# Kernel tuning notes

Measured on AMD Instinct MI355X. Metric: run time of the kernel, lower is better.

Reference implementation:

```python
import jax, jax.numpy as jnp
import numpy as np

N_NODES = 100000
N_REL = 8
N_EDGES = 80000
IN_F, HID, OUT = 128, 32, 2
N_GRAPHS = 64


def setup_inputs() -> dict:
    key = jax.random.key(0)
    ks = jax.random.split(key, 12)
    x = jax.random.normal(ks[0], (N_NODES, IN_F), dtype=jnp.float32)
    src = jax.random.randint(ks[1], (N_REL, N_EDGES), 0, N_NODES, dtype=jnp.int32)
    dst = jax.random.randint(ks[2], (N_REL, N_EDGES), 0, N_NODES, dtype=jnp.int32)
    graph_ids = jax.random.randint(ks[3], (N_NODES,), 0, N_GRAPHS, dtype=jnp.int32)
    W1 = jax.random.normal(ks[4], (N_REL, IN_F, HID), dtype=jnp.float32) / np.sqrt(IN_F)
    b1 = jnp.zeros((N_REL, HID), dtype=jnp.float32)
    W2 = jax.random.normal(ks[5], (N_REL, HID, HID), dtype=jnp.float32) / np.sqrt(HID)
    b2 = jnp.zeros((N_REL, HID), dtype=jnp.float32)
    Wc = jax.random.normal(ks[6], (HID, OUT), dtype=jnp.float32) / np.sqrt(HID)
    bc = jnp.zeros((OUT,), dtype=jnp.float32)
    return {"x": x, "src": src, "dst": dst, "graph_ids": graph_ids,
            "num_graphs": N_GRAPHS, "W1": W1, "b1": b1, "W2": W2, "b2": b2,
            "Wc": Wc, "bc": bc}


def _hetero_conv(h, src, dst, W, b, n_nodes):
    """HeteroGraphConv(sum) of per-relation GraphConv(norm='both')."""
    n_rel = W.shape[0]
    out = jnp.zeros((n_nodes, W.shape[2]), dtype=h.dtype)
    ones_e = jnp.ones((src.shape[1],), dtype=h.dtype)
    for r in range(n_rel):  # small fixed relation set
        s, d = src[r], dst[r]
        # symmetric normalization with degree clamped to >= 1 (DGL behavior)
        deg_out = jnp.maximum(jax.ops.segment_sum(ones_e, s, num_segments=n_nodes), 1.0)
        deg_in = jnp.maximum(jax.ops.segment_sum(ones_e, d, num_segments=n_nodes), 1.0)
        hn = h * jax.lax.rsqrt(deg_out)[:, None]      # [N, F_in]
        hw = hn @ W[r]                                # project first (F_in >= F_out)
        agg = jax.ops.segment_sum(hw[s], d, num_segments=n_nodes)  # scatter-sum to dst
        out = out + agg * jax.lax.rsqrt(deg_in)[:, None] + b[r]
    return out


def reference(x, src, dst, graph_ids, num_graphs, W1, b1, W2, b2, Wc, bc):
    n = x.shape[0]
    h = jax.nn.relu(_hetero_conv(x, src, dst, W1, b1, n))
    h = _hetero_conv(h, src, dst, W2, b2, n)
    # per-graph mean pooling over nodes
    sums = jax.ops.segment_sum(h, graph_ids, num_segments=num_graphs)
    cnts = jnp.maximum(jax.ops.segment_sum(jnp.ones((n,), h.dtype), graph_ids,
                                           num_segments=num_graphs), 1.0)
    pooled = sums / cnts[:, None]
    return pooled @ Wc + bc
```

## Files before the change

### kernel.cpp

```cpp
#include <hip/hip_runtime.h>


#define N_NODES 100000
#define N_REL   8
#define N_EDGES 80000
#define IN_F    128
#define HID     32
#define N_GRAPHS 64
#define NCAT    (N_REL * HID)
#define N_KEYS  (N_NODES * N_REL)
#define TOT_E   (N_REL * N_EDGES)
#define DRANGE  12500

constexpr int TILE = 256;
constexpr int KC   = 32;

typedef __attribute__((ext_vector_type(8))) short bf16x8;
typedef __attribute__((ext_vector_type(4))) float f32x4;

__device__ __forceinline__ ushort f2bf(float v) {
  unsigned u = __builtin_bit_cast(unsigned, v);
  u = (u + 0x7fffu + ((u >> 16) & 1u)) >> 16;
  return (ushort)u;
}
__device__ __forceinline__ float bf2f(ushort h) {
  unsigned u = ((unsigned)h) << 16;
  return __builtin_bit_cast(float, u);
}

__global__ __launch_bounds__(256) void deg_hist_kernel(const int* __restrict__ src, const int* __restrict__ dst,
                                                       int* __restrict__ dego, int* __restrict__ cnt) {
  int q = blockIdx.x & 7;
  int bb = blockIdx.x >> 3;
  int nb = gridDim.x >> 3;
  for (int i = bb * 256 + threadIdx.x; i < TOT_E; i += nb * 256) {
    int s = src[i], d = dst[i];
    int r = i / N_EDGES;
    if (s / DRANGE == q) atomicAdd(&dego[r * N_NODES + s], 1);
    if (d / DRANGE == q) atomicAdd(&cnt[d * N_REL + r], 1);
  }
}

__global__ __launch_bounds__(256) void rsqrt_kernel(float* __restrict__ p, int count) {
  int i = blockIdx.x * 256 + threadIdx.x;
  if (i < count) {
    int d = ((const int*)p)[i];
    p[i] = rsqrtf((float)(d < 1 ? 1 : d));
  }
}

__global__ __launch_bounds__(256) void prep_w_kernel(const float* __restrict__ W1, const float* __restrict__ W2,
                                                     const float* __restrict__ Wc,
                                                     ushort* __restrict__ Wt1, ushort* __restrict__ Vt) {
  int i = blockIdx.x * 256 + threadIdx.x;
  if (i < NCAT * IN_F) {
    int n = i >> 7, k = i & 127;
    int r = n >> 5, j = n & 31;
    Wt1[i] = f2bf(W1[r * (IN_F * HID) + k * HID + j]);
  } else {
    int q = i - NCAT * IN_F;
    if (q < 16 * HID) {
      int n = q >> 5, k = q & 31;
      int r = n >> 1, c = n & 1;
      float s = 0.f;
#pragma unroll
      for (int j = 0; j < HID; j++) s += W2[r * (HID * HID) + k * HID + j] * Wc[j * 2 + c];
      Vt[q] = f2bf(s);
    }
  }
}

__global__ __launch_bounds__(256) void scan1_kernel(const int* __restrict__ in, int* __restrict__ out,
                                                    int* __restrict__ partial, int n) {
  __shared__ int ts[256];
  int b0 = blockIdx.x * 1024;
  int t = threadIdx.x;
  int v[4]; int s = 0;
#pragma unroll
  for (int k = 0; k < 4; k++) {
    int idx = b0 + t * 4 + k;
    v[k] = s;
    s += (idx < n) ? in[idx] : 0;
  }
  ts[t] = s;
  __syncthreads();
  for (int off = 1; off < 256; off <<= 1) {
    int xv = (t >= off) ? ts[t - off] : 0;
    __syncthreads();
    ts[t] += xv;
    __syncthreads();
  }
  int texcl = (t == 0) ? 0 : ts[t - 1];
#pragma unroll
  for (int k = 0; k < 4; k++) {
    int idx = b0 + t * 4 + k;
    if (idx < n) out[idx] = texcl + v[k];
  }
  if (t == 255) partial[blockIdx.x] = ts[255];
}

__global__ __launch_bounds__(256) void scan2_kernel(int* __restrict__ partial, int nb) {
  __shared__ int ts[256];
  int t = threadIdx.x;
  int v[4]; int s = 0;
#pragma unroll
  for (int k = 0; k < 4; k++) {
    int idx = t * 4 + k;
    v[k] = s;
    s += (idx < nb) ? partial[idx] : 0;
  }
  ts[t] = s;
  __syncthreads();
  for (int off = 1; off < 256; off <<= 1) {
    int xv = (t >= off) ? ts[t - off] : 0;
    __syncthreads();
    ts[t] += xv;
    __syncthreads();
  }
  int texcl = (t == 0) ? 0 : ts[t - 1];
#pragma unroll
  for (int k = 0; k < 4; k++) {
    int idx = t * 4 + k;
    if (idx < nb) partial[idx] = texcl + v[k];
  }
}

__global__ __launch_bounds__(256) void scan3_kernel(int* __restrict__ out, const int* __restrict__ partial, int n) {
  int i = blockIdx.x * 256 + threadIdx.x;
  if (i < n) out[i] += partial[i >> 10];
  if (i == 0) out[n] = TOT_E;
}

__global__ __launch_bounds__(256) void fill_kernel(const int* __restrict__ src, const int* __restrict__ dst,
                                                   const int* __restrict__ rp, int* __restrict__ fillc,
                                                   const int* __restrict__ cnt,
                                                   int* __restrict__ ecol1, int* __restrict__ ecol2,
                                                   float* __restrict__ ew) {
  int q = blockIdx.x & 7;
  int bb = blockIdx.x >> 3;
  int nb = gridDim.x >> 3;
  for (int i = bb * 256 + threadIdx.x; i < TOT_E; i += nb * 256) {
    int d = dst[i];
    if (d / DRANGE != q) continue;
    int s = src[i];
    int r = i / N_EDGES;
    int key = d * N_REL + r;
    int c = cnt[key];
    int pos = atomicAdd(&fillc[key], 1);
    int t = rp[key] + pos;
    ecol1[t] = s * NCAT + r * HID;
    ecol2[t] = s * 16 + r * 2;
    ew[t] = rsqrtf((float)(c < 1 ? 1 : c));
  }
}

__global__ __launch_bounds__(256, 4) void gemm1_staged(const float* __restrict__ A, const ushort* __restrict__ Bt,
                                                       const float* __restrict__ rs_o, ushort* __restrict__ Y, int M) {
  __shared__ ushort smem[17408];
  int wave = __builtin_amdgcn_readfirstlane(threadIdx.x >> 6);
  int lane = threadIdx.x & 63;
  int t = threadIdx.x;
  int m0 = (blockIdx.x * 4 + wave) * 16;
  int me = (m0 <= M - 16) ? m0 : (M - 16);
  int row = lane & 15, quad = lane >> 4;

  bf16x8 af[4];
#pragma unroll
  for (int kq = 0; kq < 4; kq++) {
    const float* ap = &A[(size_t)(me + row) * IN_F + kq * 32 + quad * 8];
    float4 a0 = *(const float4*)ap;
    float4 a1 = *(const float4*)(ap + 4);
    bf16x8 a;
    a[0] = (short)f2bf(a0.x); a[1] = (short)f2bf(a0.y); a[2] = (short)f2bf(a0.z); a[3] = (short)f2bf(a0.w);
    a[4] = (short)f2bf(a1.x); a[5] = (short)f2bf(a1.y); a[6] = (short)f2bf(a1.z); a[7] = (short)f2bf(a1.w);
    af[kq] = a;
  }

  f32x4 acc[16];
#pragma unroll
  for (int nt = 0; nt < 16; nt++) acc[nt] = (f32x4){0.f, 0.f, 0.f, 0.f};

  for (int p = 0; p < 2; p++) {
    __syncthreads();
    const ushort* bsrc = Bt + (size_t)p * (128 * IN_F);
#pragma unroll
    for (int i = 0; i < 8; i++) {
      int c = t + i * 256;
      int rr2 = c >> 4, cc = c & 15;
      uint4 v = *(const uint4*)&bsrc[rr2 * IN_F + cc * 8];
      *(uint4*)&smem[rr2 * 136 + cc * 8] = v;
    }
    __syncthreads();
#pragma unroll
    for (int kq = 0; kq < 4; kq++) {
#pragma unroll
      for (int nt2 = 0; nt2 < 8; nt2++) {
        bf16x8 b = *(const bf16x8*)&smem[(nt2 * 16 + row) * 136 + kq * 32 + quad * 8];
        acc[p * 8 + nt2] = __builtin_amdgcn_mfma_f32_16x16x32_bf16(af[kq], b, acc[p * 8 + nt2], 0, 0, 0);
      }
    }
  }
  __syncthreads();

  float4 sc[N_REL];
#pragma unroll
  for (int r = 0; r < N_REL; r++)
    sc[r] = *(const float4*)&rs_o[(size_t)r * N_NODES + me + quad * 4];
  ushort* myt = &smem[wave * 4160];
#pragma unroll
  for (int nt = 0; nt < 16; nt++) {
    const float* s4 = (const float*)&sc[nt >> 1];
#pragma unroll
    for (int i = 0; i < 4; i++)
      myt[(quad * 4 + i) * 260 + nt * 16 + row] = f2bf(acc[nt][i] * s4[i]);
  }
  if (m0 <= M - 16) {
    ushort* ybase = &Y[(size_t)m0 * NCAT];
#pragma unroll
    for (int k = 0; k < 8; k++) {
      int g = k * 512 + lane * 8;
      int r2 = g >> 8, c2 = g & 255;
      const ushort* sp = &myt[r2 * 260 + c2];
      uint4 v;
      v.x = *(const uint*)(sp + 0);
      v.y = *(const uint*)(sp + 2);
      v.z = *(const uint*)(sp + 4);
      v.w = *(const uint*)(sp + 6);
      *(uint4*)&ybase[g] = v;
    }
  }
}

__global__ __launch_bounds__(256) void gemm2_mfma(const ushort* __restrict__ H, const ushort* __restrict__ Vt,
                                                  const float* __restrict__ rs_o, float* __restrict__ Ys2, int M) {
  int wave = __builtin_amdgcn_readfirstlane(threadIdx.x >> 6);
  int lane = threadIdx.x & 63;
  int m0 = (blockIdx.x * 4 + wave) * 16;
  if (m0 >= M) return;
  int row = lane & 15, quad = lane >> 4;
  f32x4 acc = (f32x4){0.f, 0.f, 0.f, 0.f};
  bf16x8 a = *(const bf16x8*)&H[(size_t)(m0 + row) * HID + quad * 8];
  bf16x8 b = *(const bf16x8*)&Vt[row * HID + quad * 8];
  acc = __builtin_amdgcn_mfma_f32_16x16x32_bf16(a, b, acc, 0, 0, 0);
  int r = row >> 1;
#pragma unroll
  for (int i = 0; i < 4; i++) {
    int m = m0 + quad * 4 + i;
    Ys2[(size_t)m * 16 + row] = acc[i] * rs_o[(size_t)r * N_NODES + m];
  }
}

__global__ __launch_bounds__(256) void gather1_kernel(const ushort* __restrict__ Ys, const int* __restrict__ ecol1,
                                                      const float* __restrict__ ew, const int* __restrict__ rp,
                                                      const float* __restrict__ b1, ushort* __restrict__ H) {
  int wave = __builtin_amdgcn_readfirstlane(threadIdx.x >> 6);
  int lane = threadIdx.x & 63;
  int d = blockIdx.x * 4 + wave;
  if (d >= N_NODES) return;
  int j = lane & 31, half = lane >> 5;
  int base = rp[d * N_REL], endp = rp[d * N_REL + N_REL];
  float sum = 0.f;
  for (int t = base + half; t < endp; t += 2) {
    int off = ecol1[t];
    float w = ew[t];
    sum += w * bf2f(Ys[(size_t)off + j]);
  }
  sum += __shfl_down(sum, 32);
  if (half == 0) {
    float sb = 0.f;
#pragma unroll
    for (int q = 0; q < N_REL; q++) sb += b1[q * HID + j];
    H[(size_t)d * HID + j] = f2bf(fmaxf(sum + sb, 0.f));
  }
}

__global__ __launch_bounds__(256) void gather2_pool_kernel(const float* __restrict__ Ys2,
                                                           const int* __restrict__ ecol2,
                                                           const float* __restrict__ ew, const int* __restrict__ rp,
                                                           const int* __restrict__ gid,
                                                           float* __restrict__ gpool, float* __restrict__ gcnt) {
  __shared__ float lp[N_GRAPHS * 2];
  __shared__ float lc[N_GRAPHS];
  int t = threadIdx.x;
  if (t < N_GRAPHS * 2) lp[t] = 0.f;
  if (t < N_GRAPHS) lc[t] = 0.f;
  __syncthreads();
  for (int n = blockIdx.x * 256 + t; n < N_NODES; n += gridDim.x * 256) {
    int base = rp[n * N_REL], endp = rp[n * N_REL + N_REL];
    float z0 = 0.f, z1 = 0.f;
    for (int s = base; s < endp; s++) {
      float w = ew[s];
      float2 y = *(const float2*)&Ys2[ecol2[s]];
      z0 += w * y.x;
      z1 += w * y.y;
    }
    int g = gid[n];
    atomicAdd(&lp[g * 2 + 0], z0);
    atomicAdd(&lp[g * 2 + 1], z1);
    atomicAdd(&lc[g], 1.f);
  }
  __syncthreads();
  if (t < N_GRAPHS * 2) atomicAdd(&gpool[t], lp[t]);
  if (t < N_GRAPHS) atomicAdd(&gcnt[t], lc[t]);
}

__global__ void final_kernel(const float* __restrict__ gpool, const float* __restrict__ gcnt,
                             const float* __restrict__ b2, const float* __restrict__ Wc,
                             const float* __restrict__ bc, float* __restrict__ out) {
  int g = threadIdx.x;
  if (g >= N_GRAPHS) return;
  float c0 = 0.f, c1 = 0.f;
#pragma unroll
  for (int k = 0; k < HID; k++) {
    float sb = 0.f;
#pragma unroll
    for (int r = 0; r < N_REL; r++) sb += b2[r * HID + k];
    c0 += sb * Wc[k * 2 + 0];
    c1 += sb * Wc[k * 2 + 1];
  }
  float cntv = gcnt[g];
  if (cntv > 0.f) {
    out[g * 2 + 0] = gpool[g * 2 + 0] / cntv + c0 + bc[0];
    out[g * 2 + 1] = gpool[g * 2 + 1] / cntv + c1 + bc[1];
  } else {
    out[g * 2 + 0] = bc[0];
    out[g * 2 + 1] = bc[1];
  }
}

__global__ __launch_bounds__(256) void deg_kernel(const int* __restrict__ src, const int* __restrict__ dst,
                                                  int* __restrict__ dego, int* __restrict__ degi, int n_rel) {
  int i = blockIdx.x * 256 + threadIdx.x;
  if (i < n_rel * N_EDGES) {
    int r = i / N_EDGES;
    atomicAdd(&dego[r * N_NODES + src[i]], 1);
    atomicAdd(&degi[r * N_NODES + dst[i]], 1);
  }
}

__global__ __launch_bounds__(256) void proj1_kernel(const float* __restrict__ x, const float* __restrict__ W1r0,
                                                    const float* __restrict__ rs_o, float* __restrict__ hw,
                                                    int n0, int n1, int hw_nodes) {
  int rr = blockIdx.y;
  int nb = n0 + blockIdx.x * TILE;
  int t = threadIdx.x;
  __shared__ float xs[TILE][KC + 4];
  const float* __restrict__ Wr = W1r0 + (size_t)rr * (IN_F * HID);
  float acc[HID];
#pragma unroll
  for (int j = 0; j < HID; j++) acc[j] = 0.f;
  for (int kc = 0; kc < IN_F; kc += KC) {
    __syncthreads();
#pragma unroll
    for (int i = 0; i < (TILE * KC / 4) / 256; i++) {
      int q = t + i * 256;
      int nn = q >> 3, k4 = q & 7;
      int n = nb + nn;
      float4 v = make_float4(0.f, 0.f, 0.f, 0.f);
      if (n < n1) v = *(const float4*)&x[(size_t)n * IN_F + kc + k4 * 4];
      *(float4*)&xs[nn][k4 * 4] = v;
    }
    __syncthreads();
#pragma unroll
    for (int k4 = 0; k4 < KC / 4; k4++) {
      float4 xv = *(const float4*)&xs[t][k4 * 4];
      const float* wk = &Wr[(kc + k4 * 4) * HID];
#pragma unroll
      for (int j = 0; j < HID; j++) acc[j] += xv.x * wk[j];
#pragma unroll
      for (int j = 0; j < HID; j++) acc[j] += xv.y * wk[HID + j];
#pragma unroll
      for (int j = 0; j < HID; j++) acc[j] += xv.z * wk[2 * HID + j];
#pragma unroll
      for (int j = 0; j < HID; j++) acc[j] += xv.w * wk[3 * HID + j];
    }
  }
  int n = nb + t;
  if (n < n1) {
    float s = rs_o[(size_t)rr * N_NODES + n];
    float* o = &hw[((size_t)rr * hw_nodes + (n - n0)) * HID];
#pragma unroll
    for (int j4 = 0; j4 < HID / 4; j4++) {
      float4 v = make_float4(acc[j4 * 4] * s, acc[j4 * 4 + 1] * s, acc[j4 * 4 + 2] * s, acc[j4 * 4 + 3] * s);
      *(float4*)&o[j4 * 4] = v;
    }
  }
}

__global__ __launch_bounds__(256) void proj2_kernel(const float* __restrict__ acc1, const float* __restrict__ b1,
                                                    const float* __restrict__ W2r0, const float* __restrict__ rs_o,
                                                    float* __restrict__ hw, int n0, int n1, int hw_nodes) {
  int n = n0 + blockIdx.x * 256 + threadIdx.x;
  if (n >= n1) return;
  int rr = blockIdx.y;
  float h1[HID];
#pragma unroll
  for (int j4 = 0; j4 < HID / 4; j4++) {
    float4 v = *(const float4*)&acc1[(size_t)n * HID + j4 * 4];
    h1[j4 * 4 + 0] = v.x; h1[j4 * 4 + 1] = v.y; h1[j4 * 4 + 2] = v.z; h1[j4 * 4 + 3] = v.w;
  }
#pragma unroll
  for (int j = 0; j < HID; j++) {
    float sb = 0.f;
#pragma unroll
    for (int q = 0; q < N_REL; q++) sb += b1[q * HID + j];
    h1[j] = fmaxf(h1[j] + sb, 0.f);
  }
  const float* __restrict__ Wr = W2r0 + (size_t)rr * (HID * HID);
  float acc[HID];
#pragma unroll
  for (int j = 0; j < HID; j++) acc[j] = 0.f;
#pragma unroll
  for (int k = 0; k < HID; k++) {
    float hv = h1[k];
#pragma unroll
    for (int j = 0; j < HID; j++) acc[j] += hv * Wr[k * HID + j];
  }
  float s = rs_o[(size_t)rr * N_NODES + n];
  float* o = &hw[((size_t)rr * hw_nodes + (n - n0)) * HID];
#pragma unroll
  for (int j4 = 0; j4 < HID / 4; j4++) {
    float4 v = make_float4(acc[j4 * 4] * s, acc[j4 * 4 + 1] * s, acc[j4 * 4 + 2] * s, acc[j4 * 4 + 3] * s);
    *(float4*)&o[j4 * 4] = v;
  }
}

__global__ __launch_bounds__(256) void scatter_kernel(const float* __restrict__ hw, const int* __restrict__ src,
                                                      const int* __restrict__ dst, const float* __restrict__ rs_i,
                                                      float* __restrict__ acc, int nr, int n0, int n1, int hw_nodes) {
  long i = (long)blockIdx.x * 256 + threadIdx.x;
  long total = (long)nr * N_EDGES * HID;
  if (i >= total) return;
  int j = (int)(i & (HID - 1));
  long e = i >> 5;
  int rr = (int)(e / N_EDGES);
  int ee = (int)(e - (long)rr * N_EDGES);
  int s = src[rr * N_EDGES + ee];
  if (s < n0 || s >= n1) return;
  int d = dst[rr * N_EDGES + ee];
  float v = hw[((size_t)rr * hw_nodes + (s - n0)) * HID + j] * rs_i[(size_t)rr * N_NODES + d];
  atomicAdd(&acc[(size_t)d * HID + j], v);
}

__global__ __launch_bounds__(256) void pool_kernel(const float* __restrict__ acc2, const float* __restrict__ b2,
                                                   const int* __restrict__ gid, float* __restrict__ gpool,
                                                   float* __restrict__ gcnt) {
  __shared__ float lp[N_GRAPHS * HID];
  __shared__ float lc[N_GRAPHS];
  int t = threadIdx.x;
  for (int i = t; i < N_GRAPHS * HID; i += 256) lp[i] = 0.f;
  if (t < N_GRAPHS) lc[t] = 0.f;
  __syncthreads();
  int j = t & (HID - 1);
  int grp = t >> 5;
  float sb = 0.f;
#pragma unroll
  for (int q = 0; q < N_REL; q++) sb += b2[q * HID + j];
  for (int n = blockIdx.x * 8 + grp; n < N_NODES; n += gridDim.x * 8) {
    int g = gid[n];
    float v = acc2[(size_t)n * HID + j] + sb;
    atomicAdd(&lp[g * HID + j], v);
    if (j == 0) atomicAdd(&lc[g], 1.f);
  }
  __syncthreads();
  for (int i = t; i < N_GRAPHS * HID; i += 256) atomicAdd(&gpool[i], lp[i]);
  if (t < N_GRAPHS) atomicAdd(&gcnt[t], lc[t]);
}

__global__ void final3_kernel(const float* __restrict__ gpool, const float* __restrict__ gcnt,
                              const float* __restrict__ Wc, const float* __restrict__ bc,
                              float* __restrict__ out) {
  int g = threadIdx.x;
  if (g >= N_GRAPHS) return;
  float inv = 1.f / fmaxf(gcnt[g], 1.f);
  float o0 = bc[0], o1 = bc[1];
#pragma unroll
  for (int k = 0; k < HID; k++) {
    float p = gpool[g * HID + k] * inv;
    o0 += p * Wc[k * 2 + 0];
    o1 += p * Wc[k * 2 + 1];
  }
  out[g * 2 + 0] = o0;
  out[g * 2 + 1] = o1;
}

extern "C" void kernel_launch(void* const* d_in, const int* in_sizes, int n_in,
                              void* d_out, int out_size, void* d_ws, size_t ws_size,
                              hipStream_t stream) {
  const float* x  = (const float*)d_in[0];
  const int* src  = (const int*)d_in[1];
  const int* dst  = (const int*)d_in[2];
  const int* gid  = (const int*)d_in[3];
  const float* W1 = (const float*)d_in[5];
  const float* b1 = (const float*)d_in[6];
  const float* W2 = (const float*)d_in[7];
  const float* b2 = (const float*)d_in[8];
  const float* Wc = (const float*)d_in[9];
  const float* bc = (const float*)d_in[10];
  float* out = (float*)d_out;

  float* ws = (float*)d_ws;
  const size_t NF = (size_t)N_NODES * HID;
  const size_t RN = (size_t)N_REL * N_NODES;
  const size_t POOLF = N_GRAPHS * HID + N_GRAPHS;
  size_t wsf = ws_size / 4;

  const size_t T1_NEED = 22500000;

  if (wsf >= T1_NEED) {
    float* gpool = ws;
    float* gcnt  = gpool + N_GRAPHS * 2;
    float* rs_o  = gcnt + N_GRAPHS;
    int*   cnt   = (int*)(rs_o + RN);
    int*   fillc = cnt + N_KEYS;
    int*   rp    = fillc + N_KEYS;
    int*   part  = rp + N_KEYS + 8;
    int*   ecol1 = part + 1024;
    int*   ecol2 = ecol1 + TOT_E;
    float* ew    = (float*)(ecol2 + TOT_E);
    float* Ys2   = ew + TOT_E;
    ushort* Ys   = (ushort*)(Ys2 + (size_t)N_NODES * 16);
    ushort* Hbf  = Ys + (size_t)N_NODES * NCAT;
    ushort* Wt1  = Hbf + (size_t)N_NODES * HID;
    ushort* Vt   = Wt1 + NCAT * IN_F;

    size_t zbytes = (N_GRAPHS * 3 + RN + 2 * (size_t)N_KEYS) * 4;
    hipMemsetAsync(ws, 0, zbytes, stream);

    deg_hist_kernel<<<1024, 256, 0, stream>>>(src, dst, (int*)rs_o, cnt);
    rsqrt_kernel<<<(int)((RN + 255) / 256), 256, 0, stream>>>(rs_o, (int)RN);
    prep_w_kernel<<<(NCAT * IN_F + 16 * HID + 255) / 256, 256, 0, stream>>>(W1, W2, Wc, Wt1, Vt);

    int sblocks = (N_KEYS + 1023) / 1024;
    scan1_kernel<<<sblocks, 256, 0, stream>>>(cnt, rp, part, N_KEYS);
    scan2_kernel<<<1, 256, 0, stream>>>(part, sblocks);
    scan3_kernel<<<(N_KEYS + 255) / 256, 256, 0, stream>>>(rp, part, N_KEYS);
    fill_kernel<<<1024, 256, 0, stream>>>(src, dst, rp, fillc, cnt, ecol1, ecol2, ew);

    int gblocks = (N_NODES / 16 + 3) / 4;
    int nblocks = (N_NODES + 3) / 4;
    gemm1_staged<<<gblocks, 256, 0, stream>>>(x, Wt1, rs_o, Ys, N_NODES);
    gather1_kernel<<<nblocks, 256, 0, stream>>>(Ys, ecol1, ew, rp, b1, Hbf);
    gemm2_mfma<<<gblocks, 256, 0, stream>>>(Hbf, Vt, rs_o, Ys2, N_NODES);
    gather2_pool_kernel<<<416, 256, 0, stream>>>(Ys2, ecol2, ew, rp, gid, gpool, gcnt);
    final_kernel<<<1, 64, 0, stream>>>(gpool, gcnt, b2, Wc, bc, out);
  } else {
    float* acc1  = ws;
    float* acc2  = acc1 + NF;
    float* gpool = acc2 + NF;
    float* gcnt  = gpool + N_GRAPHS * HID;
    float* rsb   = ws + (2 * NF + POOLF);
    size_t zf = 2 * NF + POOLF;
    float* rs_o = rsb;
    float* rs_i = rsb + N_NODES;
    float* hw = rsb + 2 * N_NODES;
    size_t fixed3 = zf + 2 * N_NODES;
    size_t avail = (wsf > fixed3) ? (wsf - fixed3) : 0;
    long chunk = (long)(avail / HID) & ~255L;
    if (chunk < 256) chunk = 256;
    if (chunk > N_NODES) chunk = N_NODES;

    size_t zb = zf * 4; if (zb > ws_size) zb = ws_size;
    hipMemsetAsync(d_ws, 0, zb, stream);

    for (int layer = 0; layer < 2; layer++) {
      for (int r = 0; r < N_REL; r++) {
        hipMemsetAsync(rs_o, 0, 2 * N_NODES * 4, stream);
        deg_kernel<<<(N_EDGES + 255) / 256, 256, 0, stream>>>(src + (size_t)r * N_EDGES, dst + (size_t)r * N_EDGES,
                                                              (int*)rs_o, (int*)rs_i, 1);
        rsqrt_kernel<<<(2 * N_NODES + 255) / 256, 256, 0, stream>>>(rs_o, 2 * N_NODES);
        for (long n0 = 0; n0 < N_NODES; n0 += chunk) {
          long n1 = n0 + chunk; if (n1 > N_NODES) n1 = N_NODES;
          int tiles = (int)((n1 - n0 + TILE - 1) / TILE);
          if (layer == 0)
            proj1_kernel<<<dim3(tiles, 1), 256, 0, stream>>>(x, W1 + (size_t)r * IN_F * HID, rs_o, hw,
                                                             (int)n0, (int)n1, (int)chunk);
          else
            proj2_kernel<<<dim3(tiles, 1), 256, 0, stream>>>(acc1, b1, W2 + (size_t)r * HID * HID, rs_o, hw,
                                                             (int)n0, (int)n1, (int)chunk);
          long tot = (long)N_EDGES * HID;
          scatter_kernel<<<(int)((tot + 255) / 256), 256, 0, stream>>>(hw, src + (size_t)r * N_EDGES,
                                                                       dst + (size_t)r * N_EDGES, rs_i,
                                                                       layer == 0 ? acc1 : acc2,
                                                                       1, (int)n0, (int)n1, (int)chunk);
        }
      }
    }
    pool_kernel<<<256, 256, 0, stream>>>(acc2, b2, gid, gpool, gcnt);
    final3_kernel<<<1, 64, 0, stream>>>(gpool, gcnt, Wc, bc, out);
  }
}
```

Measured before the change: 293.5 us.

## Partition edge atomics by physical XCD with per-XCD work queues

The degree-histogram and CSR-fill kernels now read the hardware XCC id instead of assuming that blockIdx modulo 8 maps to an XCD. Each XCD then pulls chunks of 4096 edges from its own atomic work counter and handles only the node range it owns. The goal is to keep every atomic for a given address within one XCD's L2, so relaxed, workgroup-scoped atomics can avoid cross-die coherence traffic. The cost is that correctness now depends on the hardware mapping and on workgroup-scope atomics behaving coherently across CUs of the same XCD. It also adds a dynamic queue counter that must be zeroed by the memset.

```diff
diff --git a/kernel.cpp b/kernel.cpp
--- a/kernel.cpp
+++ b/kernel.cpp
@@ -28,16 +28,37 @@
   return __builtin_bit_cast(float, u);
 }
 
+__device__ __forceinline__ unsigned phys_xcd() {
+  unsigned xcc;
+  asm volatile("s_getreg_b32 %0, hwreg(HW_REG_XCC_ID)" : "=s"(xcc));
+  return xcc & 7u;
+}
+
 __global__ __launch_bounds__(256) void deg_hist_kernel(const int* __restrict__ src, const int* __restrict__ dst,
-                                                       int* __restrict__ dego, int* __restrict__ cnt) {
-  int q = blockIdx.x & 7;
-  int bb = blockIdx.x >> 3;
-  int nb = gridDim.x >> 3;
-  for (int i = bb * 256 + threadIdx.x; i < TOT_E; i += nb * 256) {
-    int s = src[i], d = dst[i];
-    int r = i / N_EDGES;
-    if (s / DRANGE == q) atomicAdd(&dego[r * N_NODES + s], 1);
-    if (d / DRANGE == q) atomicAdd(&cnt[d * N_REL + r], 1);
+                                                       int* __restrict__ dego, int* __restrict__ cnt,
+                                                       int* __restrict__ wq) {
+  unsigned q = phys_xcd();
+  __shared__ int sbase;
+  const int CHUNK = 4096;
+  for (;;) {
+    if (threadIdx.x == 0)
+      sbase = __hip_atomic_fetch_add(&wq[q * 16], CHUNK, __ATOMIC_RELAXED, __HIP_MEMORY_SCOPE_WORKGROUP);
+    __syncthreads();
+    int base = sbase;
+    if (base >= TOT_E) break;
+#pragma unroll
+    for (int k = 0; k < 16; k++) {
+      int i = base + k * 256 + (int)threadIdx.x;
+      if (i < TOT_E) {
+        int s = src[i], d = dst[i];
+        int r = i / N_EDGES;
+        if ((unsigned)s / DRANGE == q)
+          __hip_atomic_fetch_add(&dego[r * N_NODES + s], 1, __ATOMIC_RELAXED, __HIP_MEMORY_SCOPE_WORKGROUP);
+        if ((unsigned)d / DRANGE == q)
+          __hip_atomic_fetch_add(&cnt[d * N_REL + r], 1, __ATOMIC_RELAXED, __HIP_MEMORY_SCOPE_WORKGROUP);
+      }
+    }
+    __syncthreads();
   }
 }
 
@@ -135,22 +156,33 @@
                                                    const int* __restrict__ rp, int* __restrict__ fillc,
                                                    const int* __restrict__ cnt,
                                                    int* __restrict__ ecol1, int* __restrict__ ecol2,
-                                                   float* __restrict__ ew) {
-  int q = blockIdx.x & 7;
-  int bb = blockIdx.x >> 3;
-  int nb = gridDim.x >> 3;
-  for (int i = bb * 256 + threadIdx.x; i < TOT_E; i += nb * 256) {
-    int d = dst[i];
-    if (d / DRANGE != q) continue;
-    int s = src[i];
-    int r = i / N_EDGES;
-    int key = d * N_REL + r;
-    int c = cnt[key];
-    int pos = atomicAdd(&fillc[key], 1);
-    int t = rp[key] + pos;
-    ecol1[t] = s * NCAT + r * HID;
-    ecol2[t] = s * 16 + r * 2;
-    ew[t] = rsqrtf((float)(c < 1 ? 1 : c));
+                                                   float* __restrict__ ew, int* __restrict__ wq) {
+  unsigned q = phys_xcd();
+  __shared__ int sbase;
+  const int CHUNK = 4096;
+  for (;;) {
+    if (threadIdx.x == 0)
+      sbase = __hip_atomic_fetch_add(&wq[q * 16], CHUNK, __ATOMIC_RELAXED, __HIP_MEMORY_SCOPE_WORKGROUP);
+    __syncthreads();
+    int base = sbase;
+    if (base >= TOT_E) break;
+#pragma unroll
+    for (int k = 0; k < 16; k++) {
+      int i = base + k * 256 + (int)threadIdx.x;
+      if (i >= TOT_E) continue;
+      int d = dst[i];
+      if ((unsigned)d / DRANGE != q) continue;
+      int s = src[i];
+      int r = i / N_EDGES;
+      int key = d * N_REL + r;
+      int c = cnt[key];
+      int pos = __hip_atomic_fetch_add(&fillc[key], 1, __ATOMIC_RELAXED, __HIP_MEMORY_SCOPE_WORKGROUP);
+      int t = rp[key] + pos;
+      ecol1[t] = s * NCAT + r * HID;
+      ecol2[t] = s * 16 + r * 2;
+      ew[t] = rsqrtf((float)(c < 1 ? 1 : c));
+    }
+    __syncthreads();
   }
 }
 
@@ -513,7 +545,8 @@
     float* rs_o  = gcnt + N_GRAPHS;
     int*   cnt   = (int*)(rs_o + RN);
     int*   fillc = cnt + N_KEYS;
-    int*   rp    = fillc + N_KEYS;
+    int*   wq    = fillc + N_KEYS;
+    int*   rp    = wq + 256;
     int*   part  = rp + N_KEYS + 8;
     int*   ecol1 = part + 1024;
     int*   ecol2 = ecol1 + TOT_E;
@@ -524,10 +557,10 @@
     ushort* Wt1  = Hbf + (size_t)N_NODES * HID;
     ushort* Vt   = Wt1 + NCAT * IN_F;
 
-    size_t zbytes = (N_GRAPHS * 3 + RN + 2 * (size_t)N_KEYS) * 4;
+    size_t zbytes = (N_GRAPHS * 3 + RN + 2 * (size_t)N_KEYS + 256) * 4;
     hipMemsetAsync(ws, 0, zbytes, stream);
 
-    deg_hist_kernel<<<1024, 256, 0, stream>>>(src, dst, (int*)rs_o, cnt);
+    deg_hist_kernel<<<1024, 256, 0, stream>>>(src, dst, (int*)rs_o, cnt, wq);
     rsqrt_kernel<<<(int)((RN + 255) / 256), 256, 0, stream>>>(rs_o, (int)RN);
     prep_w_kernel<<<(NCAT * IN_F + 16 * HID + 255) / 256, 256, 0, stream>>>(W1, W2, Wc, Wt1, Vt);
 
@@ -535,7 +568,7 @@
     scan1_kernel<<<sblocks, 256, 0, stream>>>(cnt, rp, part, N_KEYS);
     scan2_kernel<<<1, 256, 0, stream>>>(part, sblocks);
     scan3_kernel<<<(N_KEYS + 255) / 256, 256, 0, stream>>>(rp, part, N_KEYS);
-    fill_kernel<<<1024, 256, 0, stream>>>(src, dst, rp, fillc, cnt, ecol1, ecol2, ew);
+    fill_kernel<<<1024, 256, 0, stream>>>(src, dst, rp, fillc, cnt, ecol1, ecol2, ew, wq + 128);
 
     int gblocks = (N_NODES / 16 + 3) / 4;
     int nblocks = (N_NODES + 3) / 4;
```

After: 313.5 us. +6.8%, slower.
